# Kernel optimization log

Hardware: AMD Instinct MI355X
Metric: run time of the kernel (lower is better)

## Reference

```python
import jax, jax.numpy as jnp
import numpy as np

VOCAB = 400001  # vocab_size + 1
H = 100         # n_hidden
B = 512
T = 25
FC = 128
NC = 2
FORGET_BIAS = 1.0


def setup_inputs() -> dict:
    key = jax.random.key(0)
    ks = jax.random.split(key, 8)
    features = jax.random.randint(ks[0], (B, T), 0, VOCAB, dtype=jnp.int32)
    embedding = jax.random.normal(ks[1], (VOCAB, H), dtype=jnp.float32) * 0.05
    # BasicLSTMCell kernel: [input_dim + hidden, 4*hidden], gate order (i, j, f, o)
    k1 = jax.random.normal(ks[2], (2 * H, 4 * H), dtype=jnp.float32) * 0.05
    b1 = jnp.zeros((4 * H,), dtype=jnp.float32)
    k2 = jax.random.normal(ks[3], (2 * H, 4 * H), dtype=jnp.float32) * 0.05
    b2 = jnp.zeros((4 * H,), dtype=jnp.float32)
    w_fc1 = jax.random.normal(ks[4], (H, FC), dtype=jnp.float32) * 0.05
    b_fc1 = jnp.zeros((FC,), dtype=jnp.float32)
    w_fc2 = jax.random.normal(ks[5], (FC, NC), dtype=jnp.float32) * 0.05
    b_fc2 = jnp.zeros((NC,), dtype=jnp.float32)
    return {"features": features, "embedding": embedding,
            "k1": k1, "b1": b1, "k2": k2, "b2": b2,
            "w_fc1": w_fc1, "b_fc1": b_fc1, "w_fc2": w_fc2, "b_fc2": b_fc2}


def _lstm_cell(c, h, x, kernel, bias):
    z = jnp.concatenate([x, h], axis=-1) @ kernel + bias  # [B, 4H]
    i, j, f, o = jnp.split(z, 4, axis=-1)
    c_new = c * jax.nn.sigmoid(f + FORGET_BIAS) + jax.nn.sigmoid(i) * jnp.tanh(j)
    h_new = jnp.tanh(c_new) * jax.nn.sigmoid(o)
    return c_new, h_new


def reference(features, embedding, k1, b1, k2, b2, w_fc1, b_fc1, w_fc2, b_fc2):
    x = embedding[features]                      # [B, T, H]
    xs = jnp.swapaxes(x, 0, 1)                   # [T, B, H] for scan over time
    batch = features.shape[0]
    zeros = jnp.zeros((batch, H), dtype=embedding.dtype)

    def step(carry, xt):
        c1, h1, c2, h2 = carry
        c1, h1 = _lstm_cell(c1, h1, xt, k1, b1)
        c2, h2 = _lstm_cell(c2, h2, h1, k2, b2)
        return (c1, h1, c2, h2), None

    (c1, h1, c2, h2), _ = jax.lax.scan(step, (zeros, zeros, zeros, zeros), xs)
    # dynamic_rnn outputs[:, -1, :] == final top-layer hidden state h2
    fc1 = h2 @ w_fc1 + b_fc1                     # linear, no activation (tf.layers.dense default)
    pred = fc1 @ w_fc2 + b_fc2                   # [B, num_classes] logits
    return pred
```

## Files before the change

### kernel.cpp

```cpp
#include <hip/hip_runtime.h>
#include <cstdint>
#include <cstddef>

#define VOCABSZ 400001
#define Hn 100
#define Tn 25
#define Bn 512
#define FCn 128
#define Rr 2
#define NBLK (Bn / Rr)
#define NTHR 1024

typedef _Float16 half2_t __attribute__((ext_vector_type(2)));

__device__ __forceinline__ half2_t h2bits(unsigned v) {
    union { unsigned u; half2_t h; } x; x.u = v; return x.h;
}
__device__ __forceinline__ float fdot2f(half2_t a, half2_t b, float c) {
    return __builtin_amdgcn_fdot2(a, b, c, false);
}
__device__ __forceinline__ float sigm(float x) {
    return __fdividef(1.0f, 1.0f + __expf(-x));
}
__device__ __forceinline__ float tanh_fast(float x) {
    float e = __expf(2.0f * x);
    return __fdividef(e - 1.0f, e + 1.0f);
}

__global__ void prep_weights(const float* __restrict__ k1,
                             const float* __restrict__ k2,
                             uint4* __restrict__ WP) {
    int t = blockIdx.x * blockDim.x + threadIdx.x;
    if (t >= 2 * 25 * 400) return;
    int l   = t / 10000;
    int rem = t % 10000;
    int kq  = rem / 400;
    int o   = rem % 400;
    int u = o >> 2, g = o & 3;
    int c = g * 100 + u;
    const float* K = l ? k2 : k1;
    union { unsigned u32; half2_t h; } d[4];
    #pragma unroll
    for (int j = 0; j < 4; j++) {
        int k0 = 8 * kq + 2 * j;
        d[j].h.x = (_Float16)K[(k0    ) * 400 + c];
        d[j].h.y = (_Float16)K[(k0 + 1) * 400 + c];
    }
    uint4 v; v.x = d[0].u32; v.y = d[1].u32; v.z = d[2].u32; v.w = d[3].u32;
    WP[t] = v;
}

__device__ __forceinline__ float lstm_update(float z, int g, float& cst) {
    float t1 = __shfl_xor(z, 1);
    float t2 = __shfl_xor(z, 2);
    float t3 = __shfl_xor(t1, 2);
    bool g0 = (g & 1) != 0, g1 = (g & 2) != 0;
    float vi = g1 ? (g0 ? t3 : t2) : (g0 ? t1 : z);
    float vj = g1 ? (g0 ? t2 : t3) : (g0 ? z  : t1);
    float vf = g1 ? (g0 ? t1 : z ) : (g0 ? t3 : t2);
    float vo = g1 ? (g0 ? z  : t1) : (g0 ? t2 : t3);
    cst = cst * sigm(vf + 1.0f) + sigm(vi) * tanh_fast(vj);
    return tanh_fast(cst) * sigm(vo);
}

__device__ __forceinline__ void gemv_ds(const _Float16* __restrict__ s0,
                                        const _Float16* __restrict__ s1,
                                        const uint4* __restrict__ w,
                                        float bias, float& Z0, float& Z1) {
    const uint4* p0 = (const uint4*)s0;
    const uint4* p1 = (const uint4*)s1;
    float a0 = 0.f, a1 = 0.f, a2 = 0.f, a3 = 0.f;
    float d0 = 0.f, d1 = 0.f, d2 = 0.f, d3 = 0.f;
    #pragma unroll
    for (int kq = 0; kq < 25; kq++) {
        uint4 vx = p0[kq];
        uint4 vy = p1[kq];
        uint4 wv = w[kq];
        a0 = fdot2f(h2bits(wv.x), h2bits(vx.x), a0);
        a1 = fdot2f(h2bits(wv.y), h2bits(vx.y), a1);
        a2 = fdot2f(h2bits(wv.z), h2bits(vx.z), a2);
        a3 = fdot2f(h2bits(wv.w), h2bits(vx.w), a3);
        d0 = fdot2f(h2bits(wv.x), h2bits(vy.x), d0);
        d1 = fdot2f(h2bits(wv.y), h2bits(vy.y), d1);
        d2 = fdot2f(h2bits(wv.z), h2bits(vy.z), d2);
        d3 = fdot2f(h2bits(wv.w), h2bits(vy.w), d3);
    }
    Z0 = (a0 + a1) + (a2 + a3) + bias;
    Z1 = (d0 + d1) + (d2 + d3) + bias;
}

__global__ __launch_bounds__(NTHR, 4) void lstm_main(
    const int*   __restrict__ features,
    const float* __restrict__ embedding,
    const float* __restrict__ b1,
    const float* __restrict__ b2,
    const float* __restrict__ w_fc1,
    const float* __restrict__ b_fc1,
    const float* __restrict__ w_fc2,
    const float* __restrict__ b_fc2,
    const uint4* __restrict__ WP,
    float*       __restrict__ out)
{
    __shared__ __align__(16) _Float16 xh1[Rr][200];
    __shared__ __align__(16) _Float16 xh2[Rr][200];
    __shared__ float wred[8][2];

    const int tid  = threadIdx.x;
    const int lane = tid & 63;
    const int l    = tid >> 9;
    const int ht   = tid & 511;
    const int o    = (ht < 400) ? ht : 399;
    const int u = o >> 2, g = o & 3;
    const int c = g * 100 + u;
    const bool owner  = (ht < 400);
    const bool active = (ht < 448);

    uint4 w[25];
    #pragma unroll
    for (int kq = 0; kq < 25; kq++)
        w[kq] = WP[(l * 25 + kq) * 400 + o];

    const float bias = (l ? b2 : b1)[c];

    const _Float16* s0 = l ? &xh2[0][0] : &xh1[0][0];
    const _Float16* s1 = l ? &xh2[1][0] : &xh1[1][0];

    if (tid < 200) {
        int r = tid / 100, uu = tid % 100;
        xh1[r][100 + uu] = (_Float16)0.0f;
        xh2[r][uu]       = (_Float16)0.0f;
        xh2[r][100 + uu] = (_Float16)0.0f;
    }
    if (tid < 100) {
        int r = tid / 50, p = tid % 50;
        int f0 = features[(blockIdx.x * Rr + r) * Tn + 0];
        float2 e = *(const float2*)(embedding + (size_t)f0 * Hn + 2 * p);
        half2_t h; h.x = (_Float16)e.x; h.y = (_Float16)e.y;
        ((half2_t*)&xh1[r][0])[p] = h;
    }
    __syncthreads();

    float cst[Rr] = {0.f, 0.f};
    float hv[Rr]  = {0.f, 0.f};

    for (int ph = 0; ph <= Tn; ph++) {
        const bool dorun = active && (l ? (ph >= 1) : (ph < Tn));
        float2 epre = {0.f, 0.f};
        int prow = 0, pp = 0;
        if (dorun) {
            if (l == 0 && owner && g == 1 && ph + 1 < Tn) {
                prow = (u >= 50);
                pp   = u % 50;
                int f1 = features[(blockIdx.x * Rr + prow) * Tn + ph + 1];
                epre = *(const float2*)(embedding + (size_t)f1 * Hn + 2 * pp);
            }
            float z0, z1;
            gemv_ds(s0, s1, w, bias, z0, z1);
            hv[0] = lstm_update(z0, g, cst[0]);
            hv[1] = lstm_update(z1, g, cst[1]);
        }
        __syncthreads();
        if (l == 0 && owner && ph < Tn) {
            if (g == 0) {
                xh1[0][100 + u] = (_Float16)hv[0];
                xh1[1][100 + u] = (_Float16)hv[1];
                xh2[0][u]       = (_Float16)hv[0];
                xh2[1][u]       = (_Float16)hv[1];
            }
            if (g == 1 && ph + 1 < Tn) {
                half2_t h; h.x = (_Float16)epre.x; h.y = (_Float16)epre.y;
                ((half2_t*)&xh1[prow][0])[pp] = h;
            }
        }
        if (l == 1 && owner && ph >= 1 && g == 0) {
            xh2[0][100 + u] = (_Float16)hv[0];
            xh2[1][100 + u] = (_Float16)hv[1];
        }
        __syncthreads();
    }

    if (tid < Rr * FCn) {
        int r = tid >> 7;
        int j = tid & 127;
        float acc = b_fc1[j];
        #pragma unroll 10
        for (int uu = 0; uu < Hn; uu++)
            acc = fmaf((float)xh2[r][100 + uu], w_fc1[uu * FCn + j], acc);
        float p0 = acc * w_fc2[2 * j + 0];
        float p1 = acc * w_fc2[2 * j + 1];
        #pragma unroll
        for (int off = 32; off > 0; off >>= 1) {
            p0 += __shfl_down(p0, off, 64);
            p1 += __shfl_down(p1, off, 64);
        }
        if (lane == 0) {
            int wv = tid >> 6;
            wred[wv][0] = p0;
            wred[wv][1] = p1;
        }
    }
    __syncthreads();
    if (tid < 4) {
        int r = tid >> 1, cls = tid & 1;
        out[(blockIdx.x * Rr + r) * 2 + cls] =
            wred[2 * r][cls] + wred[2 * r + 1][cls] + b_fc2[cls];
    }
}

extern "C" void kernel_launch(void* const* d_in, const int* in_sizes, int n_in,
                              void* d_out, int out_size, void* d_ws, size_t ws_size,
                              hipStream_t stream) {
    const int*   features  = (const int*)  d_in[0];
    const float* embedding = (const float*)d_in[1];
    const float* k1        = (const float*)d_in[2];
    const float* b1        = (const float*)d_in[3];
    const float* k2        = (const float*)d_in[4];
    const float* b2        = (const float*)d_in[5];
    const float* w_fc1     = (const float*)d_in[6];
    const float* b_fc1     = (const float*)d_in[7];
    const float* w_fc2     = (const float*)d_in[8];
    const float* b_fc2     = (const float*)d_in[9];

    uint4* WP = (uint4*)d_ws;

    prep_weights<<<(20000 + 255) / 256, 256, 0, stream>>>(k1, k2, WP);
    lstm_main<<<NBLK, NTHR, 0, stream>>>(features, embedding, b1, b2,
                                         w_fc1, b_fc1, w_fc2, b_fc2,
                                         WP, (float*)d_out);
}
```

Before: 391.3 us.

## Double-buffer LSTM shared state and keep only part of the weights in registers

Shared-memory input/hidden buffers become ping-pong pairs indexed by step parity. Each layer can then write its new h (and the prefetched embedding) straight after computing it, which removes one __syncthreads per time step. The per-thread weight slice held in registers shrinks from 25 to 16 uint4. The other 9 are re-read from global memory (expected to hit cache) on every step, cutting VGPR pressure at the cost of extra memory loads on the recurrent critical path.

Measured after the change: 330.7 us. -15.5%, faster.

```diff
diff --git a/kernel.cpp b/kernel.cpp
--- a/kernel.cpp
+++ b/kernel.cpp
@@ -10,6 +10,7 @@
 #define Rr 2
 #define NBLK (Bn / Rr)
 #define NTHR 1024
+#define RKQ 16
 
 typedef _Float16 half2_t __attribute__((ext_vector_type(2)));
 
@@ -63,19 +64,34 @@
     return tanh_fast(cst) * sigm(vo);
 }
 
-__device__ __forceinline__ void gemv_ds(const _Float16* __restrict__ s0,
-                                        const _Float16* __restrict__ s1,
-                                        const uint4* __restrict__ w,
-                                        float bias, float& Z0, float& Z1) {
+__device__ __forceinline__ void gemv2(const _Float16* s0,
+                                      const _Float16* s1,
+                                      const uint4* wreg,
+                                      const uint4* __restrict__ wp,
+                                      float bias, float& Z0, float& Z1) {
     const uint4* p0 = (const uint4*)s0;
     const uint4* p1 = (const uint4*)s1;
     float a0 = 0.f, a1 = 0.f, a2 = 0.f, a3 = 0.f;
     float d0 = 0.f, d1 = 0.f, d2 = 0.f, d3 = 0.f;
     #pragma unroll
-    for (int kq = 0; kq < 25; kq++) {
+    for (int kq = RKQ; kq < 25; kq++) {
+        uint4 wv = wp[kq * 400];
         uint4 vx = p0[kq];
         uint4 vy = p1[kq];
-        uint4 wv = w[kq];
+        a0 = fdot2f(h2bits(wv.x), h2bits(vx.x), a0);
+        a1 = fdot2f(h2bits(wv.y), h2bits(vx.y), a1);
+        a2 = fdot2f(h2bits(wv.z), h2bits(vx.z), a2);
+        a3 = fdot2f(h2bits(wv.w), h2bits(vx.w), a3);
+        d0 = fdot2f(h2bits(wv.x), h2bits(vy.x), d0);
+        d1 = fdot2f(h2bits(wv.y), h2bits(vy.y), d1);
+        d2 = fdot2f(h2bits(wv.z), h2bits(vy.z), d2);
+        d3 = fdot2f(h2bits(wv.w), h2bits(vy.w), d3);
+    }
+    #pragma unroll
+    for (int kq = 0; kq < RKQ; kq++) {
+        uint4 wv = wreg[kq];
+        uint4 vx = p0[kq];
+        uint4 vy = p1[kq];
         a0 = fdot2f(h2bits(wv.x), h2bits(vx.x), a0);
         a1 = fdot2f(h2bits(wv.y), h2bits(vx.y), a1);
         a2 = fdot2f(h2bits(wv.z), h2bits(vx.z), a2);
@@ -101,8 +117,8 @@
     const uint4* __restrict__ WP,
     float*       __restrict__ out)
 {
-    __shared__ __align__(16) _Float16 xh1[Rr][200];
-    __shared__ __align__(16) _Float16 xh2[Rr][200];
+    __shared__ __align__(16) _Float16 xh1[2][Rr][200];
+    __shared__ __align__(16) _Float16 xh2[2][Rr][200];
     __shared__ float wred[8][2];
 
     const int tid  = threadIdx.x;
@@ -115,28 +131,25 @@
     const bool owner  = (ht < 400);
     const bool active = (ht < 448);
 
-    uint4 w[25];
-    #pragma unroll
-    for (int kq = 0; kq < 25; kq++)
-        w[kq] = WP[(l * 25 + kq) * 400 + o];
+    const uint4* wp = WP + (size_t)(l * 25) * 400 + o;
+    uint4 wreg[RKQ];
+    #pragma unroll
+    for (int kq = 0; kq < RKQ; kq++)
+        wreg[kq] = wp[kq * 400];
 
     const float bias = (l ? b2 : b1)[c];
-
-    const _Float16* s0 = l ? &xh2[0][0] : &xh1[0][0];
-    const _Float16* s1 = l ? &xh2[1][0] : &xh1[1][0];
 
     if (tid < 200) {
         int r = tid / 100, uu = tid % 100;
-        xh1[r][100 + uu] = (_Float16)0.0f;
-        xh2[r][uu]       = (_Float16)0.0f;
-        xh2[r][100 + uu] = (_Float16)0.0f;
+        xh1[0][r][100 + uu] = (_Float16)0.0f;
+        xh2[1][r][100 + uu] = (_Float16)0.0f;
     }
     if (tid < 100) {
         int r = tid / 50, p = tid % 50;
         int f0 = features[(blockIdx.x * Rr + r) * Tn + 0];
         float2 e = *(const float2*)(embedding + (size_t)f0 * Hn + 2 * p);
         half2_t h; h.x = (_Float16)e.x; h.y = (_Float16)e.y;
-        ((half2_t*)&xh1[r][0])[p] = h;
+        ((half2_t*)&xh1[0][r][0])[p] = h;
     }
     __syncthreads();
 
@@ -144,37 +157,40 @@
     float hv[Rr]  = {0.f, 0.f};
 
     for (int ph = 0; ph <= Tn; ph++) {
+        const int p  = ph & 1;
+        const int wb = p ^ 1;
         const bool dorun = active && (l ? (ph >= 1) : (ph < Tn));
-        float2 epre = {0.f, 0.f};
-        int prow = 0, pp = 0;
         if (dorun) {
+            float2 epre = {0.f, 0.f};
+            int prow = 0, pp = 0;
             if (l == 0 && owner && g == 1 && ph + 1 < Tn) {
                 prow = (u >= 50);
                 pp   = u % 50;
                 int f1 = features[(blockIdx.x * Rr + prow) * Tn + ph + 1];
                 epre = *(const float2*)(embedding + (size_t)f1 * Hn + 2 * pp);
             }
+            const _Float16* s0 = l ? &xh2[p][0][0] : &xh1[p][0][0];
+            const _Float16* s1 = l ? &xh2[p][1][0] : &xh1[p][1][0];
             float z0, z1;
-            gemv_ds(s0, s1, w, bias, z0, z1);
+            gemv2(s0, s1, wreg, wp, bias, z0, z1);
             hv[0] = lstm_update(z0, g, cst[0]);
             hv[1] = lstm_update(z1, g, cst[1]);
-        }
-        __syncthreads();
-        if (l == 0 && owner && ph < Tn) {
-            if (g == 0) {
-                xh1[0][100 + u] = (_Float16)hv[0];
-                xh1[1][100 + u] = (_Float16)hv[1];
-                xh2[0][u]       = (_Float16)hv[0];
-                xh2[1][u]       = (_Float16)hv[1];
+            if (l == 0 && owner) {
+                if (g == 0) {
+                    xh1[wb][0][100 + u] = (_Float16)hv[0];
+                    xh1[wb][1][100 + u] = (_Float16)hv[1];
+                    xh2[wb][0][u]       = (_Float16)hv[0];
+                    xh2[wb][1][u]       = (_Float16)hv[1];
+                }
+                if (g == 1 && ph + 1 < Tn) {
+                    half2_t h; h.x = (_Float16)epre.x; h.y = (_Float16)epre.y;
+                    ((half2_t*)&xh1[wb][prow][0])[pp] = h;
+                }
             }
-            if (g == 1 && ph + 1 < Tn) {
-                half2_t h; h.x = (_Float16)epre.x; h.y = (_Float16)epre.y;
-                ((half2_t*)&xh1[prow][0])[pp] = h;
+            if (l == 1 && owner && g == 0) {
+                xh2[wb][0][100 + u] = (_Float16)hv[0];
+                xh2[wb][1][100 + u] = (_Float16)hv[1];
             }
-        }
-        if (l == 1 && owner && ph >= 1 && g == 0) {
-            xh2[0][100 + u] = (_Float16)hv[0];
-            xh2[1][100 + u] = (_Float16)hv[1];
         }
         __syncthreads();
     }
@@ -185,7 +201,7 @@
         float acc = b_fc1[j];
         #pragma unroll 10
         for (int uu = 0; uu < Hn; uu++)
-            acc = fmaf((float)xh2[r][100 + uu], w_fc1[uu * FCn + j], acc);
+            acc = fmaf((float)xh2[0][r][100 + uu], w_fc1[uu * FCn + j], acc);
         float p0 = acc * w_fc2[2 * j + 0];
         float p1 = acc * w_fc2[2 * j + 1];
         #pragma unroll
```

## Replace per-thread fdot2 GEMV with MFMA tiles and LDS-resident weights

Applied to the files above, without the earlier changes.

The recurrent gate GEMV moves from per-thread fdot2 dot products over register-held weights to 16x16x32 f16 MFMA instructions. Each wave computes four 16-column gate tiles for the two batch rows, with the batch padded to 16 using a zero row. About 22 of the 50 weight tiles are staged in LDS and the rest are streamed from global memory. The hidden-state buffers are double-buffered, which removes one of the two barriers per step, and one wave per layer group now only prefetches the next embedding. The MFMA tile wastes 14 of 16 batch columns, and global weight reloads each step could become the new bottleneck, especially with occupancy dropped to one block per CU.

Measured after the change: 331.0 us. 1.18x faster.

```diff
diff --git a/kernel.cpp b/kernel.cpp
--- a/kernel.cpp
+++ b/kernel.cpp
@@ -2,7 +2,6 @@
 #include <cstdint>
 #include <cstddef>
 
-#define VOCABSZ 400001
 #define Hn 100
 #define Tn 25
 #define Bn 512
@@ -11,13 +10,13 @@
 #define NBLK (Bn / Rr)
 #define NTHR 1024
 
+
 typedef _Float16 half2_t __attribute__((ext_vector_type(2)));
-
-__device__ __forceinline__ half2_t h2bits(unsigned v) {
-    union { unsigned u; half2_t h; } x; x.u = v; return x.h;
-}
-__device__ __forceinline__ float fdot2f(half2_t a, half2_t b, float c) {
-    return __builtin_amdgcn_fdot2(a, b, c, false);
+typedef _Float16 f16x8  __attribute__((ext_vector_type(8)));
+typedef float    f32x4  __attribute__((ext_vector_type(4)));
+
+__device__ __forceinline__ f16x8 asf16(uint4 v) {
+    union { uint4 u; f16x8 h; } x; x.u = v; return x.h;
 }
 __device__ __forceinline__ float sigm(float x) {
     return __fdividef(1.0f, 1.0f + __expf(-x));
@@ -41,55 +40,16 @@
     const float* K = l ? k2 : k1;
     union { unsigned u32; half2_t h; } d[4];
     #pragma unroll
-    for (int j = 0; j < 4; j++) {
-        int k0 = 8 * kq + 2 * j;
-        d[j].h.x = (_Float16)K[(k0    ) * 400 + c];
-        d[j].h.y = (_Float16)K[(k0 + 1) * 400 + c];
+    for (int jj = 0; jj < 4; jj++) {
+        int k0 = 8 * kq + 2 * jj;
+        d[jj].h.x = (_Float16)K[(k0    ) * 400 + c];
+        d[jj].h.y = (_Float16)K[(k0 + 1) * 400 + c];
     }
     uint4 v; v.x = d[0].u32; v.y = d[1].u32; v.z = d[2].u32; v.w = d[3].u32;
     WP[t] = v;
 }
 
-__device__ __forceinline__ float lstm_update(float z, int g, float& cst) {
-    float t1 = __shfl_xor(z, 1);
-    float t2 = __shfl_xor(z, 2);
-    float t3 = __shfl_xor(t1, 2);
-    bool g0 = (g & 1) != 0, g1 = (g & 2) != 0;
-    float vi = g1 ? (g0 ? t3 : t2) : (g0 ? t1 : z);
-    float vj = g1 ? (g0 ? t2 : t3) : (g0 ? z  : t1);
-    float vf = g1 ? (g0 ? t1 : z ) : (g0 ? t3 : t2);
-    float vo = g1 ? (g0 ? z  : t1) : (g0 ? t2 : t3);
-    cst = cst * sigm(vf + 1.0f) + sigm(vi) * tanh_fast(vj);
-    return tanh_fast(cst) * sigm(vo);
-}
-
-__device__ __forceinline__ void gemv_ds(const _Float16* __restrict__ s0,
-                                        const _Float16* __restrict__ s1,
-                                        const uint4* __restrict__ w,
-                                        float bias, float& Z0, float& Z1) {
-    const uint4* p0 = (const uint4*)s0;
-    const uint4* p1 = (const uint4*)s1;
-    float a0 = 0.f, a1 = 0.f, a2 = 0.f, a3 = 0.f;
-    float d0 = 0.f, d1 = 0.f, d2 = 0.f, d3 = 0.f;
-    #pragma unroll
-    for (int kq = 0; kq < 25; kq++) {
-        uint4 vx = p0[kq];
-        uint4 vy = p1[kq];
-        uint4 wv = w[kq];
-        a0 = fdot2f(h2bits(wv.x), h2bits(vx.x), a0);
-        a1 = fdot2f(h2bits(wv.y), h2bits(vx.y), a1);
-        a2 = fdot2f(h2bits(wv.z), h2bits(vx.z), a2);
-        a3 = fdot2f(h2bits(wv.w), h2bits(vx.w), a3);
-        d0 = fdot2f(h2bits(wv.x), h2bits(vy.x), d0);
-        d1 = fdot2f(h2bits(wv.y), h2bits(vy.y), d1);
-        d2 = fdot2f(h2bits(wv.z), h2bits(vy.z), d2);
-        d3 = fdot2f(h2bits(wv.w), h2bits(vy.w), d3);
-    }
-    Z0 = (a0 + a1) + (a2 + a3) + bias;
-    Z1 = (d0 + d1) + (d2 + d3) + bias;
-}
-
-__global__ __launch_bounds__(NTHR, 4) void lstm_main(
+__global__ __launch_bounds__(NTHR, 1) void lstm_main(
     const int*   __restrict__ features,
     const float* __restrict__ embedding,
     const float* __restrict__ b1,
@@ -101,93 +61,147 @@
     const uint4* __restrict__ WP,
     float*       __restrict__ out)
 {
-    __shared__ __align__(16) _Float16 xh1[Rr][200];
-    __shared__ __align__(16) _Float16 xh2[Rr][200];
+    __shared__ __align__(16) uint4    WLA[22 * 400];
+    __shared__ __align__(16) _Float16 xh1[2][Rr][200];
+    __shared__ __align__(16) _Float16 xh2[2][Rr][200];
+    __shared__ __align__(16) uint4    zrow[25];
+    __shared__ __align__(16) float    bias_lds[800];
     __shared__ float wred[8][2];
 
     const int tid  = threadIdx.x;
     const int lane = tid & 63;
-    const int l    = tid >> 9;
-    const int ht   = tid & 511;
-    const int o    = (ht < 400) ? ht : 399;
-    const int u = o >> 2, g = o & 3;
-    const int c = g * 100 + u;
-    const bool owner  = (ht < 400);
-    const bool active = (ht < 448);
-
-    uint4 w[25];
-    #pragma unroll
-    for (int kq = 0; kq < 25; kq++)
-        w[kq] = WP[(l * 25 + kq) * 400 + o];
-
-    const float bias = (l ? b2 : b1)[c];
-
-    const _Float16* s0 = l ? &xh2[0][0] : &xh1[0][0];
-    const _Float16* s1 = l ? &xh2[1][0] : &xh1[1][0];
-
+    const int w    = tid >> 6;
+    const int wl   = w >> 3;
+    const int w7   = w & 7;
+    const bool workw = (w7 < 7);
+    const int q = lane >> 4;
+    const int j = lane & 15;
+
+    for (int idx = tid; idx < 22 * 400; idx += NTHR) {
+        int s   = idx / 400;
+        int rem = idx - s * 400;
+        int kq  = rem >> 4;
+        int c16 = rem & 15;
+        int l_t, ct;
+        if (s < 14) { l_t = s / 7; ct = s - l_t * 7; }
+        else        { int e = s - 14; l_t = e >> 2; ct = (e & 3) + 7; }
+        WLA[idx] = WP[(l_t * 25 + kq) * 400 + 16 * ct + c16];
+    }
+    if (tid < 800) {
+        int l_b  = tid / 400;
+        int rest = tid - l_b * 400;
+        int u = rest >> 2, g = rest & 3;
+        bias_lds[tid] = (l_b ? b2 : b1)[g * 100 + u];
+    }
+    if (tid < 25) { uint4 z; z.x = z.y = z.z = z.w = 0u; zrow[tid] = z; }
     if (tid < 200) {
         int r = tid / 100, uu = tid % 100;
-        xh1[r][100 + uu] = (_Float16)0.0f;
-        xh2[r][uu]       = (_Float16)0.0f;
-        xh2[r][100 + uu] = (_Float16)0.0f;
+        xh1[0][r][100 + uu] = (_Float16)0.f;
+        xh2[1][r][100 + uu] = (_Float16)0.f;
     }
     if (tid < 100) {
-        int r = tid / 50, p = tid % 50;
-        int f0 = features[(blockIdx.x * Rr + r) * Tn + 0];
-        float2 e = *(const float2*)(embedding + (size_t)f0 * Hn + 2 * p);
+        int r = tid / 50, pp = tid % 50;
+        int f0 = features[(blockIdx.x * Rr + r) * Tn];
+        float2 e = *(const float2*)(embedding + (size_t)f0 * Hn + 2 * pp);
         half2_t h; h.x = (_Float16)e.x; h.y = (_Float16)e.y;
-        ((half2_t*)&xh1[r][0])[p] = h;
+        ((half2_t*)&xh1[0][r][0])[pp] = h;
     }
     __syncthreads();
 
-    float cst[Rr] = {0.f, 0.f};
-    float hv[Rr]  = {0.f, 0.f};
-
+    const int ct0 = w7;
+    const int ct1 = w7 + 7;
+    const int ct2 = w7 + 14;
+    const int ct3 = w7 + 21;
+    const bool v3   = workw && (ct3 < 25);
+    const int slot0 = w7 + 7 * wl;
+    const bool t1lds = (w7 < 4);
+    const int slot1 = 14 + w7 + 4 * wl;
+    const uint4* gA = WP + (size_t)(wl * 25) * 400 + 16 * w7 + j;
+    const int bb = wl * 100;
+
+    float cst0 = 0.f, cst1 = 0.f, cst2 = 0.f, cst3 = 0.f;
+
+#define CELL(ACC, CST, CT)                                                   \
+    {                                                                        \
+        float gi = ACC[0], gj = ACC[1], gf = ACC[2], go = ACC[3];            \
+        CST = CST * sigm(gf + 1.0f) + sigm(gi) * tanh_fast(gj);              \
+        float hh = tanh_fast(CST) * sigm(go);                                \
+        if (j < 2) {                                                         \
+            _Float16 h16 = (_Float16)hh;                                     \
+            int u = 4 * (CT) + q;                                            \
+            if (wl == 0) { xh1[wb][j][100 + u] = h16;                        \
+                           xh2[wb][j][u]       = h16; }                      \
+            else           xh2[wb][j][100 + u] = h16;                        \
+        }                                                                    \
+    }
+
+    #pragma unroll 1
     for (int ph = 0; ph <= Tn; ph++) {
-        const bool dorun = active && (l ? (ph >= 1) : (ph < Tn));
-        float2 epre = {0.f, 0.f};
-        int prow = 0, pp = 0;
-        if (dorun) {
-            if (l == 0 && owner && g == 1 && ph + 1 < Tn) {
-                prow = (u >= 50);
-                pp   = u % 50;
-                int f1 = features[(blockIdx.x * Rr + prow) * Tn + ph + 1];
-                epre = *(const float2*)(embedding + (size_t)f1 * Hn + 2 * pp);
+        const int p  = ph & 1;
+        const int wb = p ^ 1;
+        if (workw) {
+            const bool dorun = wl ? (ph >= 1) : (ph < Tn);
+            if (dorun) {
+                const uint4* bbase = wl ? (const uint4*)&xh2[p][0][0]
+                                        : (const uint4*)&xh1[p][0][0];
+                const uint4* brow = (j < 2) ? (bbase + j * 25) : zrow;
+
+                f32x4 acc0 = *(const f32x4*)&bias_lds[(bb + 4 * ct0 + q) * 4];
+                f32x4 acc1 = *(const f32x4*)&bias_lds[(bb + 4 * ct1 + q) * 4];
+                f32x4 acc2 = *(const f32x4*)&bias_lds[(bb + 4 * ct2 + q) * 4];
+                f32x4 acc3;
+                if (v3) acc3 = *(const f32x4*)&bias_lds[(bb + 4 * ct3 + q) * 4];
+                else    { acc3[0]=0.f; acc3[1]=0.f; acc3[2]=0.f; acc3[3]=0.f; }
+
+                #pragma unroll
+                for (int s = 0; s < 7; s++) {
+                    const int kq = (s < 6) ? (4 * s + q) : 24;
+                    f16x8 bf;
+                    if (s < 6) bf = asf16(brow[kq]);
+                    else {
+                        const uint4* b6 = (q == 0) ? brow : zrow;
+                        bf = asf16(b6[24]);
+                    }
+                    f16x8 a0 = asf16(WLA[slot0 * 400 + kq * 16 + j]);
+                    acc0 = __builtin_amdgcn_mfma_f32_16x16x32_f16(a0, bf, acc0, 0, 0, 0);
+                    f16x8 a1;
+                    if (t1lds) a1 = asf16(WLA[slot1 * 400 + kq * 16 + j]);
+                    else       a1 = asf16(gA[kq * 400 + 112]);
+                    acc1 = __builtin_amdgcn_mfma_f32_16x16x32_f16(a1, bf, acc1, 0, 0, 0);
+                    f16x8 a2 = asf16(gA[kq * 400 + 224]);
+                    acc2 = __builtin_amdgcn_mfma_f32_16x16x32_f16(a2, bf, acc2, 0, 0, 0);
+                    if (v3) {
+                        f16x8 a3 = asf16(gA[kq * 400 + 336]);
+                        acc3 = __builtin_amdgcn_mfma_f32_16x16x32_f16(a3, bf, acc3, 0, 0, 0);
+                    }
+                }
+                CELL(acc0, cst0, ct0);
+                CELL(acc1, cst1, ct1);
+                CELL(acc2, cst2, ct2);
+                if (v3) CELL(acc3, cst3, ct3);
             }
-            float z0, z1;
-            gemv_ds(s0, s1, w, bias, z0, z1);
-            hv[0] = lstm_update(z0, g, cst[0]);
-            hv[1] = lstm_update(z1, g, cst[1]);
+        } else {
+            int pid = lane + (wl << 6);
+            if (pid < 100 && ph + 1 < Tn) {
+                int r = pid / 50, pp = pid % 50;
+                int f1 = features[(blockIdx.x * Rr + r) * Tn + ph + 1];
+                float2 e = *(const float2*)(embedding + (size_t)f1 * Hn + 2 * pp);
+                half2_t hv; hv.x = (_Float16)e.x; hv.y = (_Float16)e.y;
+                ((half2_t*)&xh1[wb][r][0])[pp] = hv;
+            }
         }
         __syncthreads();
-        if (l == 0 && owner && ph < Tn) {
-            if (g == 0) {
-                xh1[0][100 + u] = (_Float16)hv[0];
-                xh1[1][100 + u] = (_Float16)hv[1];
-                xh2[0][u]       = (_Float16)hv[0];
-                xh2[1][u]       = (_Float16)hv[1];
-            }
-            if (g == 1 && ph + 1 < Tn) {
-                half2_t h; h.x = (_Float16)epre.x; h.y = (_Float16)epre.y;
-                ((half2_t*)&xh1[prow][0])[pp] = h;
-            }
-        }
-        if (l == 1 && owner && ph >= 1 && g == 0) {
-            xh2[0][100 + u] = (_Float16)hv[0];
-            xh2[1][100 + u] = (_Float16)hv[1];
-        }
-        __syncthreads();
     }
 
     if (tid < Rr * FCn) {
-        int r = tid >> 7;
-        int j = tid & 127;
-        float acc = b_fc1[j];
+        int r  = tid >> 7;
+        int jj = tid & 127;
+        float acc = b_fc1[jj];
         #pragma unroll 10
         for (int uu = 0; uu < Hn; uu++)
-            acc = fmaf((float)xh2[r][100 + uu], w_fc1[uu * FCn + j], acc);
-        float p0 = acc * w_fc2[2 * j + 0];
-        float p1 = acc * w_fc2[2 * j + 1];
+            acc = fmaf((float)xh2[0][r][100 + uu], w_fc1[uu * FCn + jj], acc);
+        float p0 = acc * w_fc2[2 * jj + 0];
+        float p1 = acc * w_fc2[2 * jj + 1];
         #pragma unroll
         for (int off = 32; off > 0; off >>= 1) {
             p0 += __shfl_down(p0, off, 64);
@@ -205,6 +219,7 @@
         out[(blockIdx.x * Rr + r) * 2 + cls] =
             wred[2 * r][cls] + wred[2 * r + 1][cls] + b_fc2[cls];
     }
+#undef CELL
 }
 
 extern "C" void kernel_launch(void* const* d_in, const int* in_sizes, int n_in,
```
